# Optimization experiments

Hardware: AMD Instinct MI355X
Metric: run time of the kernel (lower is better)

## Reference

```python
import jax, jax.numpy as jnp
import numpy as np

B, T, D, L, G = 64, 256, 1024, 2, 128


def _sn(W, u):
    # torch.nn.utils.spectral_norm: one power iteration, u/v detached
    u = u / (jnp.linalg.norm(u) + 1e-12)
    v = W.T @ u
    v = v / (jnp.linalg.norm(v) + 1e-12)
    u2 = W @ v
    u2 = u2 / (jnp.linalg.norm(u2) + 1e-12)
    u2 = jax.lax.stop_gradient(u2)
    v = jax.lax.stop_gradient(v)
    return W / (u2 @ (W @ v))


def _cell(x, h, c, Wih, Whh, b):
    gates = x @ Wih.T + h @ Whh.T + b  # [B,4D]; torch gate order i,f,g,o
    i, f, g, o = jnp.split(gates, 4, axis=-1)
    c = jax.nn.sigmoid(f) * c + jax.nn.sigmoid(i) * jnp.tanh(g)
    h = jax.nn.sigmoid(o) * jnp.tanh(c)
    return h, c


def _encoder(x, Wih, Whh, b):
    inp = jnp.swapaxes(x, 0, 1)  # [T,B,D]
    bs = x.shape[0]
    hs, cs = [], []
    for l in range(L):
        W1, W2, bb = Wih[l], Whh[l], b[l]

        def step(carry, xt, W1=W1, W2=W2, bb=bb):
            h, c = _cell(xt, carry[0], carry[1], W1, W2, bb)
            return (h, c), h

        init = (jnp.zeros((bs, D), x.dtype), jnp.zeros((bs, D), x.dtype))
        (hL, cL), inp = jax.lax.scan(step, init, inp)
        hs.append(hL)
        cs.append(cL)
    return jnp.stack(hs), jnp.stack(cs)  # [L,B,D] each


def _vae(h, muW, mub, sgW, sgb, outW, outb, eps):
    mu = jnp.einsum('lbd,lgd->lbg', h, muW) + mub[:, None, :]
    sg = jnp.einsum('lbd,lgd->lbg', h, sgW) + sgb[:, None, :]
    z = mu + eps * jnp.exp(sg)  # reparameterization trick
    out = jnp.einsum('lbg,ldg->lbd', z, outW) + outb[:, None, :]
    return out, mu, sg


def _decoder(init_x, h, c, Wih, Whh, b, length):
    def step(carry, _):
        prev, h, c = carry
        x = prev
        nh, nc = [], []
        for l in range(L):
            hl, cl = _cell(x, h[l], c[l], Wih[l], Whh[l], b[l])
            nh.append(hl)
            nc.append(cl)
            x = hl
        return (x, jnp.stack(nh), jnp.stack(nc)), x

    _, ys = jax.lax.scan(step, (init_x, h, c), None, length=length)
    return jnp.swapaxes(ys, 0, 1)  # [B,T,D]


def setup_inputs() -> dict:
    key = jax.random.key(0)
    ks = iter(jax.random.split(key, 40))
    sD = 1.0 / np.sqrt(D)
    sG = 1.0 / np.sqrt(G)

    def uni(shape, s):
        return jax.random.uniform(next(ks), shape, jnp.float32, -s, s)

    inp = {
        'x': jax.random.normal(next(ks), (B, T, D), jnp.float32),
        'initial': jnp.zeros((1, D), jnp.float32),
        'enc_Wih': uni((L, 4 * D, D), sD), 'enc_Whh': uni((L, 4 * D, D), sD),
        'enc_b': uni((L, 4 * D), sD),
        'enc_u_ih': jax.random.normal(next(ks), (L, 4 * D), jnp.float32),
        'enc_u_hh': jax.random.normal(next(ks), (L, 4 * D), jnp.float32),
        'dec_Wih': uni((L, 4 * D, D), sD), 'dec_Whh': uni((L, 4 * D, D), sD),
        'dec_b': uni((L, 4 * D), sD),
        'dec_u_ih': jax.random.normal(next(ks), (L, 4 * D), jnp.float32),
        'dec_u_hh': jax.random.normal(next(ks), (L, 4 * D), jnp.float32),
        'h_muW': uni((L, G, D), sD), 'h_mub': uni((L, G), sD),
        'h_sgW': uni((L, G, D), sD), 'h_sgb': uni((L, G), sD),
        'h_outW': uni((L, D, G), sG), 'h_outb': uni((L, D), sG),
        'c_muW': uni((L, G, D), sD), 'c_mub': uni((L, G), sD),
        'c_sgW': uni((L, G, D), sD), 'c_sgb': uni((L, G), sD),
        'c_outW': uni((L, D, G), sG), 'c_outb': uni((L, D), sG),
        'eps_h': jax.random.normal(next(ks), (L, B, G), jnp.float32),
        'eps_c': jax.random.normal(next(ks), (L, B, G), jnp.float32),
    }
    return inp


def reference(x, initial, enc_Wih, enc_Whh, enc_b, enc_u_ih, enc_u_hh,
              dec_Wih, dec_Whh, dec_b, dec_u_ih, dec_u_hh,
              h_muW, h_mub, h_sgW, h_sgb, h_outW, h_outb,
              c_muW, c_mub, c_sgW, c_sgb, c_outW, c_outb,
              eps_h, eps_c):
    # spectral-norm reparam of all recurrent weight matrices (per layer)
    eW1 = jax.vmap(_sn)(enc_Wih, enc_u_ih)
    eW2 = jax.vmap(_sn)(enc_Whh, enc_u_hh)
    dW1 = jax.vmap(_sn)(dec_Wih, dec_u_ih)
    dW2 = jax.vmap(_sn)(dec_Whh, dec_u_hh)
    h, c = _encoder(x, eW1, eW2, enc_b)
    h, h_mu, h_sg = _vae(h, h_muW, h_mub, h_sgW, h_sgb, h_outW, h_outb, eps_h)
    c, c_mu, c_sg = _vae(c, c_muW, c_mub, c_sgW, c_sgb, c_outW, c_outb, eps_c)
    init_x = jnp.broadcast_to(initial, (x.shape[0], D))
    out = _decoder(init_x, h, c, dW1, dW2, dec_b, x.shape[1])
    mu = jnp.concatenate([h_mu, c_mu], axis=0)
    sg = jnp.concatenate([h_sg, c_sg], axis=0)
    return out, mu, sg
```

## Files before the change

### kernel.cpp

```cpp
#include <hip/hip_runtime.h>

#define B_  64
#define T_  256
#define D_  1024
#define G_  128
#define FD  4096
#define K2  2048
#define BD  65536
#define NWG 256
#define CL  128

typedef unsigned short u16;
typedef __attribute__((ext_vector_type(8))) short frag8;
typedef __attribute__((ext_vector_type(4))) float f4;
typedef __attribute__((ext_vector_type(4))) int i4;

__device__ __forceinline__ u16 f2b(float f) {
  unsigned u = __float_as_uint(f);
  u += 0x7fffu + ((u >> 16) & 1u);
  return (u16)(u >> 16);
}
__device__ __forceinline__ float b2f(u16 s) {
  return __uint_as_float(((unsigned)s) << 16);
}
__device__ __forceinline__ float sigm(float x) { return 1.0f / (1.0f + __expf(-x)); }

__device__ __forceinline__ void stcoh4(void* p, i4 w) {
  asm volatile("global_store_dwordx4 %0, %1, off sc0 sc1"
               :: "v"(p), "v"(w) : "memory");
}

__device__ __forceinline__ void poll4_pub(const unsigned* s, int base,
                                          unsigned tgt, unsigned* lf,
                                          unsigned val) {
  const int l = threadIdx.x & 63;
  for (;;) {
    bool ok = true;
    if (l < 4)
      ok = __hip_atomic_load(&s[(base + l) * CL], __ATOMIC_RELAXED,
                             __HIP_MEMORY_SCOPE_AGENT) >= tgt;
    if (__all(ok)) break;
    __builtin_amdgcn_s_sleep(1);
  }
  if (l == 0)
    __hip_atomic_store(lf, val, __ATOMIC_RELAXED, __HIP_MEMORY_SCOPE_WORKGROUP);
  asm volatile("" ::: "memory");
}

__device__ __forceinline__ void lds_wait(const unsigned* lf, unsigned seq) {
  while (__hip_atomic_load(lf, __ATOMIC_RELAXED,
                           __HIP_MEMORY_SCOPE_WORKGROUP) < seq)
    __builtin_amdgcn_s_sleep(1);
  asm volatile("" ::: "memory");
}

__device__ __forceinline__ void wg_arrive(unsigned* cnt, int line) {
  asm volatile("s_waitcnt vmcnt(0)" ::: "memory");
  __syncthreads();
  if (threadIdx.x == 0)
    __hip_atomic_fetch_add(&cnt[line * CL], 1u, __ATOMIC_RELAXED,
                           __HIP_MEMORY_SCOPE_AGENT);
}

__device__ __forceinline__ void wave_wait16(const unsigned* cnt, unsigned tgt) {
  const int l = threadIdx.x & 63;
  if (l < 16) {
    while (__hip_atomic_load(&cnt[l * CL], __ATOMIC_RELAXED,
                             __HIP_MEMORY_SCOPE_AGENT) < tgt)
      __builtin_amdgcn_s_sleep(2);
  }
  asm volatile("" ::: "memory");
}

__device__ __forceinline__ void fullsync(unsigned* g, unsigned ep, int wg,
                                         bool fenced) {
  if (fenced) __builtin_amdgcn_fence(__ATOMIC_RELEASE, "agent");
  wg_arrive(g, wg & 15);
  wave_wait16(g, ep * 16u);
  __syncthreads();
  if (fenced) {
    __builtin_amdgcn_fence(__ATOMIC_ACQUIRE, "agent");
    __syncthreads();
  }
}

__device__ __forceinline__ void load_weights(const u16* __restrict__ Wg, char* wlds) {
  const int t  = threadIdx.x;
  const int r  = t >> 4;
  const int c0 = t & 15;
  const char* src = (const char*)(Wg + (long)r * K2);
  char* dstrow = wlds + (r << 12);
  const int swz = (r & 7) << 4;
  #pragma unroll
  for (int i = 0; i < 16; ++i) {
    const int cb = (c0 + (i << 4)) << 4;
    frag8 v = *(const frag8*)(src + cb);
    *(frag8*)(dstrow + (cb ^ swz)) = v;
  }
  __syncthreads();
}

__device__ __forceinline__ void cellw(
    const u16* __restrict__ A0, const unsigned* c0p, unsigned t0,
    const u16* __restrict__ A1, const unsigned* c1p, unsigned t1,
    const char* wlds, float* gl, unsigned* lsf, unsigned seq,
    float& c_reg, const f4& bias, int ug0,
    u16* __restrict__ hout, float* __restrict__ fout, long fstride)
{
  const int tid = threadIdx.x;
  const int lane = tid & 63, wv = tid >> 6;
  const int mt = wv & 3, kh = wv >> 2;
  const int l15 = lane & 15, lgr = lane >> 4;

  f4 acc0 = (f4){0.f,0.f,0.f,0.f}, acc1 = (f4){0.f,0.f,0.f,0.f};
  const u16* Ab = kh ? A1 : A0;
  const unsigned* cp = kh ? c1p : c0p;
  const unsigned tg  = kh ? t1 : t0;
  unsigned* lf = lsf + kh;
  if (Ab) {
    const u16* apb = Ab + (lgr * 64 + mt * 16 + l15) * 8;
    const int kbyte0 = (kh << 11) + (lgr << 4);
    const int swz = (l15 & 7) << 4;
    const char* w0r = wlds + ((long)l15 << 12);
    const char* w1r = wlds + ((long)(16 + l15) << 12);
    if (cp) {
      const unsigned fb = 4u * (seq - 1u);
      #pragma unroll
      for (int cc = 0; cc < 4; ++cc) {
        if (mt == 0) poll4_pub(cp, cc * 4, tg, lf, fb + (unsigned)cc + 1u);
        else         lds_wait(lf, fb + (unsigned)cc + 1u);
        #pragma unroll
        for (int kk = cc * 8; kk < cc * 8 + 8; ++kk) {
          frag8 af = *(const frag8*)(apb + kk * 2048);
          const int kb = (kbyte0 + (kk << 6)) ^ swz;
          frag8 b0 = *(const frag8*)(w0r + kb);
          frag8 b1 = *(const frag8*)(w1r + kb);
          acc0 = __builtin_amdgcn_mfma_f32_16x16x32_bf16(af, b0, acc0, 0, 0, 0);
          acc1 = __builtin_amdgcn_mfma_f32_16x16x32_bf16(af, b1, acc1, 0, 0, 0);
        }
      }
    } else {
      #pragma unroll 8
      for (int kk = 0; kk < 32; ++kk) {
        frag8 af = *(const frag8*)(apb + kk * 2048);
        const int kb = (kbyte0 + (kk << 6)) ^ swz;
        frag8 b0 = *(const frag8*)(w0r + kb);
        frag8 b1 = *(const frag8*)(w1r + kb);
        acc0 = __builtin_amdgcn_mfma_f32_16x16x32_bf16(af, b0, acc0, 0, 0, 0);
        acc1 = __builtin_amdgcn_mfma_f32_16x16x32_bf16(af, b1, acc1, 0, 0, 0);
      }
    }
  }
  float* g = gl + kh * (64 * 32);
  const int orow = mt * 16 + lgr * 4;
  #pragma unroll
  for (int r = 0; r < 4; ++r) {
    g[(orow + r) * 32 + l15]      = acc0[r];
    g[(orow + r) * 32 + 16 + l15] = acc1[r];
  }
  __syncthreads();

  const int row = tid >> 3, ul = tid & 7;
  f4 p0 = *(const f4*)(gl + row * 32 + ul * 4);
  f4 p1 = *(const f4*)(gl + 64 * 32 + row * 32 + ul * 4);
  float iv = p0.x + p1.x + bias.x;
  float fv = p0.y + p1.y + bias.y;
  float gv = p0.z + p1.z + bias.z;
  float ov = p0.w + p1.w + bias.w;
  float cn = sigm(fv) * c_reg + sigm(iv) * tanhf(gv);
  float hh = sigm(ov) * tanhf(cn);
  c_reg = cn;
  unsigned hv = (unsigned)f2b(hh);
  unsigned a  = hv | (__shfl_xor(hv, 1) << 16);
  unsigned b  = __shfl_xor(a, 2);
  unsigned c2 = __shfl_xor(a, 4);
  unsigned d2 = __shfl_xor(b, 4);
  if (ul == 0) {
    i4 w; w.x = (int)a; w.y = (int)b; w.z = (int)c2; w.w = (int)d2;
    stcoh4(hout + ug0 * 64 + row * 8, w);
  }
  if (fout) fout[(long)row * fstride + ug0 + ul] = hh;
}

__device__ __forceinline__ void vae_wg(
    int bid, char* scr,
    const u16* h0f, const u16* h1f, const float* c0f, const float* c1f,
    const float* hmuW, const float* hmub, const float* hsgW, const float* hsgb,
    const float* houtW, const float* houtb,
    const float* cmuW, const float* cmub, const float* csgW, const float* csgb,
    const float* coutW, const float* coutb,
    const float* eps_h, const float* eps_c,
    float* muo, float* sgo, u16* hd0, u16* hd1, float* cd0, float* cd1)
{
  float* hrow = (float*)scr;
  float* muv  = hrow + 1024;
  float* sgv  = muv + 128;
  float* zz   = sgv + 128;
  const int tid = threadIdx.x;
  const int b = bid & 63, l = (bid >> 6) & 1, s = bid >> 7;

  if (s == 0) {
    const u16* h = l ? h1f : h0f;
    for (int i = tid; i < D_; i += 512)
      hrow[i] = b2f(h[(i >> 3) * 512 + b * 8 + (i & 7)]);
  } else {
    const float* c = (l ? c1f : c0f) + b * D_;
    for (int i = tid; i < D_; i += 512) hrow[i] = c[i];
  }
  __syncthreads();

  const float* muW = (s ? cmuW : hmuW) + (long)l * G_ * D_;
  const float* sgW = (s ? csgW : hsgW) + (long)l * G_ * D_;
  const float* mub = (s ? cmub : hmub) + l * G_;
  const float* sgb = (s ? csgb : hsgb) + l * G_;
  const int wv = tid >> 6, lane = tid & 63;
  for (int oi = wv; oi < 2 * G_; oi += 8) {
    const int g = (oi < G_) ? oi : oi - G_;
    const float* Wr = ((oi < G_) ? muW : sgW) + (long)g * D_;
    float d = 0.f;
    for (int j = lane; j < D_; j += 64) d += Wr[j] * hrow[j];
    for (int off = 1; off < 64; off <<= 1) d += __shfl_xor(d, off);
    if (lane == 0) {
      if (oi < G_) muv[g] = d + mub[g]; else sgv[g] = d + sgb[g];
    }
  }
  __syncthreads();
  if (tid < G_) {
    const int g = tid;
    const float mu = muv[g], sg = sgv[g];
    const float* ep = (s ? eps_c : eps_h) + ((long)l * B_ + b) * G_;
    zz[g] = mu + ep[g] * __expf(sg);
    muo[(long)bid * G_ + g] = mu;
    sgo[(long)bid * G_ + g] = sg;
  }
  __syncthreads();
  const float* oW  = (s ? coutW : houtW) + (long)l * D_ * G_;
  const float* obv = (s ? coutb : houtb) + l * D_;
  for (int i = 0; i < 2; ++i) {
    const int dd = i * 512 + tid;
    float acc = obv[dd];
    const float* Wr = oW + (long)dd * G_;
    #pragma unroll 4
    for (int g = 0; g < G_; ++g) acc += zz[g] * Wr[g];
    if (s == 0) {
      (l ? hd1 : hd0)[(dd >> 3) * 512 + b * 8 + (dd & 7)] = f2b(acc);
    } else {
      (l ? cd1 : cd0)[b * D_ + dd] = acc;
    }
  }
  __syncthreads();
}

__global__ __launch_bounds__(512, 1)
void persist(const u16* __restrict__ Wpe, const u16* __restrict__ Wpd,
             const float* __restrict__ bp,
             const u16* __restrict__ xb, const u16* __restrict__ xd0,
             u16* ring0, u16* ring1,
             float* ce0, float* ce1,
             u16* hd0i, u16* hd1i, float* cd0, float* cd1,
             const float* hmuW, const float* hmub, const float* hsgW, const float* hsgb,
             const float* houtW, const float* houtb,
             const float* cmuW, const float* cmub, const float* csgW, const float* csgb,
             const float* coutW, const float* coutb,
             const float* eps_h, const float* eps_c,
             float* out, float* muo, float* sgo, unsigned* bar)
{
  __shared__ __align__(16) char smem[147456 + 64];
  char*  wlds = smem;
  float* gl   = (float*)(smem + 131072);
  unsigned* lsf = (unsigned*)(smem + 147456);

  unsigned* gcnt = bar;
  unsigned* acnt = bar + 2048;
  unsigned* bcnt = bar + 4096;
  unsigned* ccnt = bar + 6144;
  unsigned* dcnt = bar + 8192;

  const int wg  = blockIdx.x;
  const bool isL0 = (wg < 128);
  const int wgL = wg & 127;
  const int ug0 = wgL * 8;
  const int tid = threadIdx.x;
  const int aline = wgL >> 3;

  if (tid == 0) { lsf[0] = 0; lsf[1] = 0; }
  load_weights(Wpe + (isL0 ? 0l : (long)FD * K2) + (long)wgL * 32 * K2, wlds);
  f4 bias = *(const f4*)(bp + (isL0 ? 0 : FD) + (ug0 + (tid & 7)) * 4);
  float c_reg = 0.f;

  if (isL0) {
    for (int s = 0; s < T_; ++s) {
      cellw(xb + (long)s * BD, nullptr, 0,
            s ? (ring0 + (long)(s - 1) * BD) : nullptr,
            s ? acnt : nullptr, 8u * (unsigned)s,
            wlds, gl, lsf, (unsigned)(s + 1),
            c_reg, bias, ug0,
            ring0 + (long)s * BD, nullptr, 0);
      wg_arrive(acnt, aline);
    }
  } else {
    for (int t = 0; t < T_; ++t) {
      cellw(ring0 + (long)t * BD, acnt, 8u * (unsigned)(t + 1),
            t ? (ring1 + (long)(t - 1) * BD) : nullptr,
            t ? bcnt : nullptr, 8u * (unsigned)t,
            wlds, gl, lsf, (unsigned)(t + 1),
            c_reg, bias, ug0,
            ring1 + (long)t * BD, nullptr, 0);
      wg_arrive(bcnt, aline);
    }
  }
  {
    const int row = tid >> 3, ul = tid & 7;
    (isL0 ? ce0 : ce1)[row * D_ + ug0 + ul] = c_reg;
  }
  fullsync(gcnt, 1, wg, true);

  vae_wg(wg, (char*)gl,
         ring0 + 255l * BD, ring1 + 255l * BD, ce0, ce1,
         hmuW, hmub, hsgW, hsgb, houtW, houtb,
         cmuW, cmub, csgW, csgb, coutW, coutb,
         eps_h, eps_c, muo, sgo, hd0i, hd1i, cd0, cd1);
  fullsync(gcnt, 2, wg, true);

  if (tid == 0) { lsf[0] = 0; lsf[1] = 0; }
  load_weights(Wpd + (isL0 ? 0l : (long)FD * K2) + (long)wgL * 32 * K2, wlds);
  bias = *(const f4*)(bp + 2 * FD + (isL0 ? 0 : FD) + (ug0 + (tid & 7)) * 4);
  {
    const int row = tid >> 3, ul = tid & 7;
    c_reg = (isL0 ? cd0 : cd1)[row * D_ + ug0 + ul];
  }

  if (isL0) {
    for (int t = 0; t < T_; ++t) {
      cellw(t ? (ring1 + (long)(t - 1) * BD) : xd0,
            t ? dcnt : nullptr, 8u * (unsigned)t,
            t ? (ring0 + (long)(t - 1) * BD) : hd0i,
            t ? ccnt : nullptr, 8u * (unsigned)t,
            wlds, gl, lsf, (unsigned)(t + 1),
            c_reg, bias, ug0,
            ring0 + (long)t * BD, nullptr, 0);
      wg_arrive(ccnt, aline);
    }
  } else {
    for (int t = 0; t < T_; ++t) {
      cellw(ring0 + (long)t * BD, ccnt, 8u * (unsigned)(t + 1),
            t ? (ring1 + (long)(t - 1) * BD) : hd1i,
            t ? dcnt : nullptr, 8u * (unsigned)t,
            wlds, gl, lsf, (unsigned)(t + 1),
            c_reg, bias, ug0,
            ring1 + (long)t * BD, out + (long)t * D_, (long)T_ * D_);
      wg_arrive(dcnt, aline);
    }
  }
}

__device__ __forceinline__ const float* selW(int m, const float* a, const float* b,
                                             const float* c, const float* d) {
  const float* W;
  switch (m >> 1) { case 0: W = a; break; case 1: W = b; break;
                    case 2: W = c; break; default: W = d; }
  return W + (long)(m & 1) * FD * D_;
}
__device__ __forceinline__ const float* selU(int m, const float* a, const float* b,
                                             const float* c, const float* d) {
  const float* u;
  switch (m >> 1) { case 0: u = a; break; case 1: u = b; break;
                    case 2: u = c; break; default: u = d; }
  return u + (m & 1) * FD;
}

__global__ __launch_bounds__(256)
void k_unorm(const float* euih, const float* euhh, const float* duih, const float* duhh,
             float* uinv)
{
  const int m = blockIdx.x;
  const float* u = selU(m, euih, euhh, duih, duhh);
  float s = 0.f;
  for (int i = threadIdx.x; i < FD; i += 256) { float v = u[i]; s += v * v; }
  __shared__ float red[4];
  for (int off = 1; off < 64; off <<= 1) s += __shfl_xor(s, off);
  if ((threadIdx.x & 63) == 0) red[threadIdx.x >> 6] = s;
  __syncthreads();
  if (threadIdx.x == 0)
    uinv[m] = 1.0f / (sqrtf(red[0] + red[1] + red[2] + red[3]) + 1e-12f);
}

__global__ __launch_bounds__(256)
void k_v(const float* eWih, const float* eWhh, const float* dWih, const float* dWhh,
         const float* euih, const float* euhh, const float* duih, const float* duhh,
         const float* uinv, float* v, float* vss)
{
  __shared__ float us[FD];
  __shared__ float red[4];
  const int m = blockIdx.x >> 2, cb = blockIdx.x & 3;
  const float* W = selW(m, eWih, eWhh, dWih, dWhh);
  const float* u = selU(m, euih, euhh, duih, duhh);
  for (int i = threadIdx.x; i < FD; i += 256) us[i] = u[i];
  __syncthreads();
  const int j = cb * 256 + threadIdx.x;
  float acc = 0.f;
  for (int i = 0; i < FD; ++i) acc += W[(long)i * D_ + j] * us[i];
  acc *= uinv[m];
  v[m * D_ + j] = acc;
  float s = acc * acc;
  for (int off = 1; off < 64; off <<= 1) s += __shfl_xor(s, off);
  if ((threadIdx.x & 63) == 0) red[threadIdx.x >> 6] = s;
  __syncthreads();
  if (threadIdx.x == 0) vss[blockIdx.x] = red[0] + red[1] + red[2] + red[3];
}

__global__ __launch_bounds__(256)
void k_sig(const float* eWih, const float* eWhh, const float* dWih, const float* dWhh,
           const float* v, float* sgp)
{
  __shared__ float vl[D_];
  __shared__ float red[4];
  const int m = blockIdx.x >> 6, rb = blockIdx.x & 63;
  const float* W = selW(m, eWih, eWhh, dWih, dWhh);
  for (int i = threadIdx.x; i < D_; i += 256) vl[i] = v[m * D_ + i];
  __syncthreads();
  const int wv = threadIdx.x >> 6, lane = threadIdx.x & 63;
  float ssq = 0.f;
  for (int rr = 0; rr < 16; ++rr) {
    const int r = rb * 64 + wv * 16 + rr;
    const float* Wr = W + (long)r * D_;
    float d = 0.f;
    for (int j = lane; j < D_; j += 64) d += Wr[j] * vl[j];
    for (int off = 1; off < 64; off <<= 1) d += __shfl_xor(d, off);
    ssq += d * d;
  }
  if (lane == 0) red[wv] = ssq;
  __syncthreads();
  if (threadIdx.x == 0) sgp[blockIdx.x] = red[0] + red[1] + red[2] + red[3];
}

__global__ void k_fin(const float* vss, const float* sgp, float* rsig)
{
  const int m = threadIdx.x;
  if (m < 8) {
    float vn = sqrtf(vss[m * 4] + vss[m * 4 + 1] + vss[m * 4 + 2] + vss[m * 4 + 3]);
    float s2 = 0.f;
    for (int i = 0; i < 64; ++i) s2 += sgp[m * 64 + i];
    rsig[m] = (vn + 1e-12f) / sqrtf(s2);
  }
}

__global__ __launch_bounds__(256)
void k_pack(const float* eWih, const float* eWhh, const float* dWih, const float* dWhh,
            const float* rsig, u16* Wpe, u16* Wpd)
{
  const long idx = (long)blockIdx.x * 256 + threadIdx.x;
  const int k8   = (int)(idx & 255);
  const int np   = (int)((idx >> 8) & 4095);
  const int pair = (int)(idx >> 20);
  const int l = pair & 1, ed = pair >> 1;
  const int u = np >> 2, g = np & 3;
  const int srow = g * D_ + u;
  const int k = k8 * 8;
  const float* src; float sc;
  if (k < D_) {
    const float* Wih = ed ? dWih : eWih;
    src = Wih + ((long)(l * FD + srow)) * D_ + k;
    sc  = rsig[ed ? 4 + l : l];
  } else {
    const float* Whh = ed ? dWhh : eWhh;
    src = Whh + ((long)(l * FD + srow)) * D_ + (k - D_);
    sc  = rsig[ed ? 6 + l : 2 + l];
  }
  f4 a = *(const f4*)src;
  f4 b = *(const f4*)(src + 4);
  frag8 o;
  o[0] = (short)f2b(a.x * sc); o[1] = (short)f2b(a.y * sc);
  o[2] = (short)f2b(a.z * sc); o[3] = (short)f2b(a.w * sc);
  o[4] = (short)f2b(b.x * sc); o[5] = (short)f2b(b.y * sc);
  o[6] = (short)f2b(b.z * sc); o[7] = (short)f2b(b.w * sc);
  u16* dst = (ed ? Wpd : Wpe) + ((long)(l * FD + np)) * K2 + k;
  *(frag8*)dst = o;
}

__global__ void k_packb(const float* eb, const float* db, float* bp)
{
  const int idx = blockIdx.x * 256 + threadIdx.x;
  const int j = idx & 4095, pair = idx >> 12;
  const int l = pair & 1, ed = pair >> 1;
  const float* b = (ed ? db : eb) + l * FD;
  bp[pair * FD + j] = b[(j & 3) * D_ + (j >> 2)];
}

__global__ __launch_bounds__(512)
void k_xb(const float* __restrict__ x, u16* __restrict__ xb)
{
  const long i8 = ((long)blockIdx.x * 512 + threadIdx.x) * 8;
  const int t   = (int)(i8 >> 16);
  const int rem = (int)(i8 & 65535);
  const int m   = rem >> 9;
  const int b   = (rem >> 3) & 63;
  const float* src = x + ((long)b * T_ + t) * D_ + m * 8;
  f4 a = *(const f4*)src;
  f4 c = *(const f4*)(src + 4);
  frag8 o;
  o[0] = (short)f2b(a.x); o[1] = (short)f2b(a.y);
  o[2] = (short)f2b(a.z); o[3] = (short)f2b(a.w);
  o[4] = (short)f2b(c.x); o[5] = (short)f2b(c.y);
  o[6] = (short)f2b(c.z); o[7] = (short)f2b(c.w);
  *(frag8*)(xb + i8) = o;
}

__global__ __launch_bounds__(512)
void k_xd0(const float* __restrict__ initial, u16* __restrict__ xd0)
{
  const int i8 = (blockIdx.x * 512 + threadIdx.x) * 8;
  const int m  = i8 >> 9;
  f4 a = *(const f4*)(initial + m * 8);
  f4 c = *(const f4*)(initial + m * 8 + 4);
  frag8 o;
  o[0] = (short)f2b(a.x); o[1] = (short)f2b(a.y);
  o[2] = (short)f2b(a.z); o[3] = (short)f2b(a.w);
  o[4] = (short)f2b(c.x); o[5] = (short)f2b(c.y);
  o[6] = (short)f2b(c.z); o[7] = (short)f2b(c.w);
  *(frag8*)(xd0 + i8) = o;
}

extern "C" void kernel_launch(void* const* d_in, const int* in_sizes, int n_in,
                              void* d_out, int out_size, void* d_ws, size_t ws_size,
                              hipStream_t stream)
{
  const float* x       = (const float*)d_in[0];
  const float* initial = (const float*)d_in[1];
  const float* eWih    = (const float*)d_in[2];
  const float* eWhh    = (const float*)d_in[3];
  const float* eb      = (const float*)d_in[4];
  const float* euih    = (const float*)d_in[5];
  const float* euhh    = (const float*)d_in[6];
  const float* dWih    = (const float*)d_in[7];
  const float* dWhh    = (const float*)d_in[8];
  const float* db      = (const float*)d_in[9];
  const float* duih    = (const float*)d_in[10];
  const float* duhh    = (const float*)d_in[11];
  const float* hmuW    = (const float*)d_in[12];
  const float* hmub    = (const float*)d_in[13];
  const float* hsgW    = (const float*)d_in[14];
  const float* hsgb    = (const float*)d_in[15];
  const float* houtW   = (const float*)d_in[16];
  const float* houtb   = (const float*)d_in[17];
  const float* cmuW    = (const float*)d_in[18];
  const float* cmub    = (const float*)d_in[19];
  const float* csgW    = (const float*)d_in[20];
  const float* csgb    = (const float*)d_in[21];
  const float* coutW   = (const float*)d_in[22];
  const float* coutb   = (const float*)d_in[23];
  const float* eps_h   = (const float*)d_in[24];
  const float* eps_c   = (const float*)d_in[25];

  char* w = (char*)d_ws;
  auto alloc = [&](size_t n) -> char* {
    char* p = w; w += (n + 255) & ~(size_t)255; return p;
  };
  u16*   Wpe   = (u16*)  alloc(2l * FD * K2 * 2);
  u16*   Wpd   = (u16*)  alloc(2l * FD * K2 * 2);
  u16*   xb    = (u16*)  alloc((long)T_ * BD * 2);
  u16*   ring0 = (u16*)  alloc((long)T_ * BD * 2);
  u16*   ring1 = (u16*)  alloc((long)T_ * BD * 2);
  u16*   xd0   = (u16*)  alloc((long)BD * 2);
  u16*   hd0i  = (u16*)  alloc((long)BD * 2);
  u16*   hd1i  = (u16*)  alloc((long)BD * 2);
  float* ce0   = (float*)alloc((long)BD * 4);
  float* ce1   = (float*)alloc((long)BD * 4);
  float* cd0   = (float*)alloc((long)BD * 4);
  float* cd1   = (float*)alloc((long)BD * 4);
  float* bp    = (float*)alloc(4l * FD * 4);
  float* vv    = (float*)alloc(8l * D_ * 4);
  float* uinv  = (float*)alloc(64);
  float* vss   = (float*)alloc(256);
  float* sgp   = (float*)alloc(4096);
  float* rsig  = (float*)alloc(64);
  unsigned* bar = (unsigned*)alloc(40960);

  hipMemsetAsync(bar, 0, 40960, stream);

  k_unorm<<<8,    256, 0, stream>>>(euih, euhh, duih, duhh, uinv);
  k_v    <<<32,   256, 0, stream>>>(eWih, eWhh, dWih, dWhh, euih, euhh, duih, duhh,
                                    uinv, vv, vss);
  k_sig  <<<512,  256, 0, stream>>>(eWih, eWhh, dWih, dWhh, vv, sgp);
  k_fin  <<<1,    64,  0, stream>>>(vss, sgp, rsig);
  k_pack <<<16384,256, 0, stream>>>(eWih, eWhh, dWih, dWhh, rsig, Wpe, Wpd);
  k_packb<<<64,   256, 0, stream>>>(eb, db, bp);
  k_xb   <<<4096, 512, 0, stream>>>(x, xb);
  k_xd0  <<<16,   512, 0, stream>>>(initial, xd0);

  float* out = (float*)d_out;
  float* muo = out + (long)B_ * T_ * D_;
  float* sgo = muo + 4l * B_ * G_;

  persist<<<NWG, 512, 0, stream>>>(Wpe, Wpd, bp, xb, xd0,
                                   ring0, ring1,
                                   ce0, ce1, hd0i, hd1i, cd0, cd1,
                                   hmuW, hmub, hsgW, hsgb, houtW, houtb,
                                   cmuW, cmub, csgW, csgb, coutW, coutb,
                                   eps_h, eps_c, out, muo, sgo, bar);
}
```

Measured before the change: 5.914 ms.

## Split LSTM cell K-reduction across both operands per wave group with finer polling

Each wave group now processes half of both input operands' K range instead of one group owning the whole input half and the other the recurrent half. The operand already available (A1) is multiplied first, and the operand produced by the other layer (A0) is consumed in finer chunks, polled two counters at a time. This is meant to let every wave start work immediately and overlap waiting on cross-workgroup producers with useful MFMA work, balancing load between the two groups. It adds a 16-counter poll and an extra LDS flag, and it swaps the operand order for layer 0 of the encoder.

```diff
diff --git a/kernel.cpp b/kernel.cpp
--- a/kernel.cpp
+++ b/kernel.cpp
@@ -30,14 +30,30 @@
                :: "v"(p), "v"(w) : "memory");
 }
 
-__device__ __forceinline__ void poll4_pub(const unsigned* s, int base,
+__device__ __forceinline__ void poll2_pub(const unsigned* s, int base,
                                           unsigned tgt, unsigned* lf,
                                           unsigned val) {
   const int l = threadIdx.x & 63;
   for (;;) {
     bool ok = true;
-    if (l < 4)
+    if (l < 2)
       ok = __hip_atomic_load(&s[(base + l) * CL], __ATOMIC_RELAXED,
+                             __HIP_MEMORY_SCOPE_AGENT) >= tgt;
+    if (__all(ok)) break;
+    __builtin_amdgcn_s_sleep(1);
+  }
+  if (l == 0)
+    __hip_atomic_store(lf, val, __ATOMIC_RELAXED, __HIP_MEMORY_SCOPE_WORKGROUP);
+  asm volatile("" ::: "memory");
+}
+
+__device__ __forceinline__ void poll16_pub(const unsigned* s, unsigned tgt,
+                                           unsigned* lf, unsigned val) {
+  const int l = threadIdx.x & 63;
+  for (;;) {
+    bool ok = true;
+    if (l < 16)
+      ok = __hip_atomic_load(&s[l * CL], __ATOMIC_RELAXED,
                              __HIP_MEMORY_SCOPE_AGENT) >= tgt;
     if (__all(ok)) break;
     __builtin_amdgcn_s_sleep(1);
@@ -101,7 +117,7 @@
 }
 
 __device__ __forceinline__ void cellw(
-    const u16* __restrict__ A0, const unsigned* c0p, unsigned t0,
+    const u16* __restrict__ A0, const unsigned* c0p, unsigned t0, int a0half,
     const u16* __restrict__ A1, const unsigned* c1p, unsigned t1,
     const char* wlds, float* gl, unsigned* lsf, unsigned seq,
     float& c_reg, const f4& bias, int ug0,
@@ -109,49 +125,56 @@
 {
   const int tid = threadIdx.x;
   const int lane = tid & 63, wv = tid >> 6;
-  const int mt = wv & 3, kh = wv >> 2;
+  const int mt = wv & 3, ks = wv >> 2;
   const int l15 = lane & 15, lgr = lane >> 4;
 
   f4 acc0 = (f4){0.f,0.f,0.f,0.f}, acc1 = (f4){0.f,0.f,0.f,0.f};
-  const u16* Ab = kh ? A1 : A0;
-  const unsigned* cp = kh ? c1p : c0p;
-  const unsigned tg  = kh ? t1 : t0;
-  unsigned* lf = lsf + kh;
-  if (Ab) {
-    const u16* apb = Ab + (lgr * 64 + mt * 16 + l15) * 8;
-    const int kbyte0 = (kh << 11) + (lgr << 4);
-    const int swz = (l15 & 7) << 4;
-    const char* w0r = wlds + ((long)l15 << 12);
-    const char* w1r = wlds + ((long)(16 + l15) << 12);
-    if (cp) {
+  const int lbase = (lgr * 64 + mt * 16 + l15) * 8;
+  const int kwb = lgr << 4;
+  const int swz = (l15 & 7) << 4;
+  const char* w0r = wlds + ((long)l15 << 12);
+  const char* w1r = wlds + ((long)(16 + l15) << 12);
+  const int kk0 = ks * 16;
+
+#define MM1(AP, HB, KK) {                                                      \
+    frag8 af = *(const frag8*)((AP) + lbase + (KK) * 2048);                    \
+    const int kb = ((HB) + ((KK) << 6) + kwb) ^ swz;                           \
+    frag8 b0 = *(const frag8*)(w0r + kb);                                      \
+    frag8 b1 = *(const frag8*)(w1r + kb);                                      \
+    acc0 = __builtin_amdgcn_mfma_f32_16x16x32_bf16(af, b0, acc0, 0, 0, 0);     \
+    acc1 = __builtin_amdgcn_mfma_f32_16x16x32_bf16(af, b1, acc1, 0, 0, 0); }
+
+  if (A1) {
+    const int hb1 = (1 - a0half) << 11;
+    if (c1p) {
+      if (wv == 0) poll16_pub(c1p, t1, &lsf[2], seq);
+      else         lds_wait(&lsf[2], seq);
+    }
+    #pragma unroll 8
+    for (int kk = kk0; kk < kk0 + 16; ++kk) MM1(A1, hb1, kk)
+  }
+  if (A0) {
+    const int hb0 = a0half << 11;
+    if (c0p) {
       const unsigned fb = 4u * (seq - 1u);
+      unsigned* lf = &lsf[ks];
       #pragma unroll
-      for (int cc = 0; cc < 4; ++cc) {
-        if (mt == 0) poll4_pub(cp, cc * 4, tg, lf, fb + (unsigned)cc + 1u);
-        else         lds_wait(lf, fb + (unsigned)cc + 1u);
+      for (int cl = 0; cl < 4; ++cl) {
+        const int cc = ks * 4 + cl;
+        const unsigned val = fb + (unsigned)cl + 1u;
+        if (mt == 0) poll2_pub(c0p, cc * 2, t0, lf, val);
+        else         lds_wait(lf, val);
         #pragma unroll
-        for (int kk = cc * 8; kk < cc * 8 + 8; ++kk) {
-          frag8 af = *(const frag8*)(apb + kk * 2048);
-          const int kb = (kbyte0 + (kk << 6)) ^ swz;
-          frag8 b0 = *(const frag8*)(w0r + kb);
-          frag8 b1 = *(const frag8*)(w1r + kb);
-          acc0 = __builtin_amdgcn_mfma_f32_16x16x32_bf16(af, b0, acc0, 0, 0, 0);
-          acc1 = __builtin_amdgcn_mfma_f32_16x16x32_bf16(af, b1, acc1, 0, 0, 0);
-        }
+        for (int kk = cc * 4; kk < cc * 4 + 4; ++kk) MM1(A0, hb0, kk)
       }
     } else {
       #pragma unroll 8
-      for (int kk = 0; kk < 32; ++kk) {
-        frag8 af = *(const frag8*)(apb + kk * 2048);
-        const int kb = (kbyte0 + (kk << 6)) ^ swz;
-        frag8 b0 = *(const frag8*)(w0r + kb);
-        frag8 b1 = *(const frag8*)(w1r + kb);
-        acc0 = __builtin_amdgcn_mfma_f32_16x16x32_bf16(af, b0, acc0, 0, 0, 0);
-        acc1 = __builtin_amdgcn_mfma_f32_16x16x32_bf16(af, b1, acc1, 0, 0, 0);
-      }
-    }
-  }
-  float* g = gl + kh * (64 * 32);
+      for (int kk = kk0; kk < kk0 + 16; ++kk) MM1(A0, hb0, kk)
+    }
+  }
+#undef MM1
+
+  float* g = gl + ks * (64 * 32);
   const int orow = mt * 16 + lgr * 4;
   #pragma unroll
   for (int r = 0; r < 4; ++r) {
@@ -283,16 +306,16 @@
   const int tid = threadIdx.x;
   const int aline = wgL >> 3;
 
-  if (tid == 0) { lsf[0] = 0; lsf[1] = 0; }
+  if (tid == 0) { lsf[0] = 0; lsf[1] = 0; lsf[2] = 0; }
   load_weights(Wpe + (isL0 ? 0l : (long)FD * K2) + (long)wgL * 32 * K2, wlds);
   f4 bias = *(const f4*)(bp + (isL0 ? 0 : FD) + (ug0 + (tid & 7)) * 4);
   float c_reg = 0.f;
 
   if (isL0) {
     for (int s = 0; s < T_; ++s) {
-      cellw(xb + (long)s * BD, nullptr, 0,
-            s ? (ring0 + (long)(s - 1) * BD) : nullptr,
-            s ? acnt : nullptr, 8u * (unsigned)s,
+      cellw(s ? (ring0 + (long)(s - 1) * BD) : nullptr,
+            s ? acnt : nullptr, 8u * (unsigned)s, 1,
+            xb + (long)s * BD, nullptr, 0,
             wlds, gl, lsf, (unsigned)(s + 1),
             c_reg, bias, ug0,
             ring0 + (long)s * BD, nullptr, 0);
@@ -300,7 +323,7 @@
     }
   } else {
     for (int t = 0; t < T_; ++t) {
-      cellw(ring0 + (long)t * BD, acnt, 8u * (unsigned)(t + 1),
+      cellw(ring0 + (long)t * BD, acnt, 8u * (unsigned)(t + 1), 0,
             t ? (ring1 + (long)(t - 1) * BD) : nullptr,
             t ? bcnt : nullptr, 8u * (unsigned)t,
             wlds, gl, lsf, (unsigned)(t + 1),
@@ -322,7 +345,7 @@
          eps_h, eps_c, muo, sgo, hd0i, hd1i, cd0, cd1);
   fullsync(gcnt, 2, wg, true);
 
-  if (tid == 0) { lsf[0] = 0; lsf[1] = 0; }
+  if (tid == 0) { lsf[0] = 0; lsf[1] = 0; lsf[2] = 0; }
   load_weights(Wpd + (isL0 ? 0l : (long)FD * K2) + (long)wgL * 32 * K2, wlds);
   bias = *(const f4*)(bp + 2 * FD + (isL0 ? 0 : FD) + (ug0 + (tid & 7)) * 4);
   {
@@ -333,7 +356,7 @@
   if (isL0) {
     for (int t = 0; t < T_; ++t) {
       cellw(t ? (ring1 + (long)(t - 1) * BD) : xd0,
-            t ? dcnt : nullptr, 8u * (unsigned)t,
+            t ? dcnt : nullptr, 8u * (unsigned)t, 0,
             t ? (ring0 + (long)(t - 1) * BD) : hd0i,
             t ? ccnt : nullptr, 8u * (unsigned)t,
             wlds, gl, lsf, (unsigned)(t + 1),
@@ -343,7 +366,7 @@
     }
   } else {
     for (int t = 0; t < T_; ++t) {
-      cellw(ring0 + (long)t * BD, ccnt, 8u * (unsigned)(t + 1),
+      cellw(ring0 + (long)t * BD, ccnt, 8u * (unsigned)(t + 1), 0,
             t ? (ring1 + (long)(t - 1) * BD) : hd1i,
             t ? dcnt : nullptr, 8u * (unsigned)t,
             wlds, gl, lsf, (unsigned)(t + 1),
```

After: 5.021 ms. 15.1% less time.
